# Optimization experiments

Measured on AMD Instinct MI355X. Metric: run time of the kernel, lower is better.

## Reference

```python
import jax, jax.numpy as jnp
import numpy as np

D_MODEL = 1024
N_HEAD = 16
HEAD_DIM = D_MODEL // N_HEAD


def setup_inputs() -> dict:
    key = jax.random.key(0)
    ks = jax.random.split(key, 11)
    B, S = 2, 2048
    scale = 1.0 / np.sqrt(D_MODEL)
    inp = {
        'q': jax.random.normal(ks[0], (B, S, D_MODEL), dtype=jnp.float32),
        'k': jax.random.normal(ks[1], (B, S, D_MODEL), dtype=jnp.float32),
        'v': jax.random.normal(ks[2], (B, S, D_MODEL), dtype=jnp.float32),
        'Wq': jax.random.normal(ks[3], (D_MODEL, D_MODEL), dtype=jnp.float32) * scale,
        'bq': jnp.zeros((D_MODEL,), dtype=jnp.float32),
        'Wk': jax.random.normal(ks[4], (D_MODEL, D_MODEL), dtype=jnp.float32) * scale,
        'bk': jnp.zeros((D_MODEL,), dtype=jnp.float32),
        'Wv': jax.random.normal(ks[5], (D_MODEL, D_MODEL), dtype=jnp.float32) * scale,
        'bv': jnp.zeros((D_MODEL,), dtype=jnp.float32),
        'Wo': jax.random.normal(ks[6], (D_MODEL, D_MODEL), dtype=jnp.float32) * scale,
        'bo': jnp.zeros((D_MODEL,), dtype=jnp.float32),
    }
    return inp


def _split_heads(x):
    # [B, S, D] -> [B, H, S, Dh]
    B, S, _ = x.shape
    return x.reshape(B, S, N_HEAD, HEAD_DIM).transpose(0, 2, 1, 3)


def reference(q, k, v, Wq, bq, Wk, bk, Wv, bv, Wo, bo):
    B, S, _ = q.shape
    qh = _split_heads(q @ Wq + bq)  # [B,H,S,Dh]
    kh = _split_heads(k @ Wk + bk)
    vh = _split_heads(v @ Wv + bv)
    inv_sqrt_d = jnp.asarray(1.0 / np.sqrt(HEAD_DIM), dtype=q.dtype)
    scores = jnp.einsum('bhqd,bhkd->bhqk', qh, kh) * inv_sqrt_d  # [B,H,S,S]
    attn = jax.nn.softmax(scores, axis=-1)
    out = jnp.einsum('bhqk,bhkd->bhqd', attn, vh)  # [B,H,S,Dh]
    out = out.transpose(0, 2, 1, 3).reshape(B, S, D_MODEL)
    return out @ Wo + bo
```

## Files before the change

kernel.cpp:

```cpp
#include <hip/hip_runtime.h>
#include <cstdint>
#include <cstddef>

#define D_MODEL 1024
#define NHEAD 16
#define HDIM 64
#define BATCH 2
#define SEQ 2048
#define MROWS (BATCH*SEQ)

typedef _Float16 f16;
typedef _Float16 f16x2 __attribute__((ext_vector_type(2)));
typedef _Float16 f16x4 __attribute__((ext_vector_type(4)));
typedef _Float16 f16x8 __attribute__((ext_vector_type(8)));
typedef float f32x4 __attribute__((ext_vector_type(4)));
typedef __fp16 fp16x2_raw __attribute__((ext_vector_type(2)));

__device__ __forceinline__ f16x2 cvt_pk(float a, float b) {
  fp16x2_raw t = __builtin_amdgcn_cvt_pkrtz(a, b);
  return __builtin_bit_cast(f16x2, t);
}

__device__ __forceinline__ float fast_exp2(float x) {
  return __builtin_amdgcn_exp2f(x);
}

#define QSCALE 0.18033688011112042f
#define CSHIFT 6.0f

__device__ __forceinline__ void gload_lds16(const void* gsrc, void* ldst) {
  __builtin_amdgcn_global_load_lds(
      (__attribute__((address_space(1))) void*)gsrc,
      (__attribute__((address_space(3))) void*)ldst,
      16, 0, 0);
}

__global__ __launch_bounds__(256) void cast3_kernel(
    const float* __restrict__ q, const float* __restrict__ k,
    const float* __restrict__ v, f16* __restrict__ Xf) {
  const int z = blockIdx.y;
  const float* in = (z == 0) ? q : (z == 1) ? k : v;
  f16* out = Xf + (size_t)z * MROWS * D_MODEL;
  int i = (blockIdx.x * 256 + threadIdx.x) * 8;
  const float4* p = (const float4*)(in + i);
  float4 a = p[0], b = p[1];
  f16x8 o = { (f16)a.x,(f16)a.y,(f16)a.z,(f16)a.w,
              (f16)b.x,(f16)b.y,(f16)b.z,(f16)b.w };
  *(f16x8*)(out + i) = o;
}

__global__ __launch_bounds__(256) void transpose4_kernel(
    const float* __restrict__ W0, const float* __restrict__ W1,
    const float* __restrict__ W2, const float* __restrict__ W3,
    f16* __restrict__ T0, f16* __restrict__ T1,
    f16* __restrict__ T2, f16* __restrict__ T3) {
  const int z = blockIdx.z;
  const float* W = (z == 0) ? W0 : (z == 1) ? W1 : (z == 2) ? W2 : W3;
  f16* Wt = (z == 0) ? T0 : (z == 1) ? T1 : (z == 2) ? T2 : T3;
  __shared__ float tile[32][33];
  int n0 = blockIdx.x * 32, k0 = blockIdx.y * 32;
  int tx = threadIdx.x, ty = threadIdx.y;
  #pragma unroll
  for (int j = 0; j < 32; j += 8)
    tile[ty + j][tx] = W[(size_t)(k0 + ty + j) * D_MODEL + n0 + tx];
  __syncthreads();
  #pragma unroll
  for (int j = 0; j < 32; j += 8)
    Wt[(size_t)(n0 + ty + j) * D_MODEL + k0 + tx] = (f16)tile[tx][ty + j];
}

__global__ __launch_bounds__(256, 3) void gemm_qkv(
    const f16* __restrict__ Xf,
    const f16* __restrict__ Wtq, const f16* __restrict__ Wtk, const f16* __restrict__ Wtv,
    const float* __restrict__ bq, const float* __restrict__ bk, const float* __restrict__ bv,
    f16* __restrict__ Qh, f16* __restrict__ Kf, f16* __restrict__ Vf) {
  __shared__ __align__(16) f16 As[128 * 64];
  __shared__ __align__(16) f16 Bs[128 * 64];
  const int id = blockIdx.x;
  const int xcd = id & 7;
  const int s5 = id >> 3;
  const int bn_i = s5 & 7;
  const int t5 = xcd * 12 + (s5 >> 3);
  const int z = t5 >> 5;
  const int bm_i = t5 & 31;
  const int bm = bm_i * 128, bn = bn_i * 128;
  const f16* A  = Xf + (size_t)z * MROWS * D_MODEL + (size_t)bm * 1024;
  const f16* Bt = ((z == 0) ? Wtq : (z == 1) ? Wtk : Wtv) + (size_t)bn * 1024;
  const float* bias = (z == 0) ? bq : (z == 1) ? bk : bv;
  const int tid = threadIdx.x, wave = tid >> 6, lane = tid & 63;
  const int lr = lane & 15, lq = lane >> 4, sw = lr & 7;
  const int wm = (wave >> 1) * 64, wn = (wave & 1) * 64;
  const int srow = lane >> 3;
  const int scs  = (lane & 7) ^ srow;
  const f16* Ag = A  + (size_t)(wave * 32 + srow) * 1024 + scs * 8;
  const f16* Bg = Bt + (size_t)(wave * 32 + srow) * 1024 + scs * 8;

  f32x4 acc[4][4];
  #pragma unroll
  for (int i = 0; i < 4; i++)
    #pragma unroll
    for (int j = 0; j < 4; j++) acc[i][j] = (f32x4){0.f, 0.f, 0.f, 0.f};

  for (int k0 = 0; k0 < 1024; k0 += 64) {
    __syncthreads();
    #pragma unroll
    for (int g = 0; g < 4; g++) {
      gload_lds16(Ag + (size_t)g * 8 * 1024 + k0, As + wave * 2048 + g * 512);
      gload_lds16(Bg + (size_t)g * 8 * 1024 + k0, Bs + wave * 2048 + g * 512);
    }
    __syncthreads();
    #pragma unroll
    for (int t = 0; t < 2; t++) {
      f16x8 af[4], bf[4];
      #pragma unroll
      for (int m = 0; m < 4; m++)
        af[m] = *(const f16x8*)(As + (size_t)(wm + m * 16 + lr) * 64 + (((t * 4 + lq) ^ sw) * 8));
      #pragma unroll
      for (int j = 0; j < 4; j++)
        bf[j] = *(const f16x8*)(Bs + (size_t)(wn + j * 16 + lr) * 64 + (((t * 4 + lq) ^ sw) * 8));
      #pragma unroll
      for (int m = 0; m < 4; m++)
        #pragma unroll
        for (int j = 0; j < 4; j++)
          acc[m][j] = __builtin_amdgcn_mfma_f32_16x16x32_f16(af[m], bf[j], acc[m][j], 0, 0, 0);
    }
  }

  #pragma unroll
  for (int j = 0; j < 4; j++) {
    const int col = bn + wn + j * 16 + lr;
    const float bj = bias[col];
    const int hh = col >> 6, d = col & 63;
    #pragma unroll
    for (int m = 0; m < 4; m++) {
      #pragma unroll
      for (int r = 0; r < 4; r++) {
        const int row = bm + wm + m * 16 + lq * 4 + r;
        float val = acc[m][j][r] + bj;
        if (z == 0) val *= QSCALE;
        const int b = row >> 11, s = row & 2047;
        const size_t bh = (size_t)b * NHEAD + hh;
        const int tile = s >> 6;
        if (z == 0) {
          Qh[(bh * SEQ + s) * HDIM + d] = (f16)val;
        } else if (z == 1) {
          const int kk = s & 63;
          const int f = ((kk >> 4) << 1) | (d >> 5);
          const int ln = ((d >> 3) & 3) * 16 + (kk & 15);
          Kf[((bh * 32 + tile) * 8 + f) * 512 + ln * 8 + (d & 7)] = (f16)val;
        } else {
          const int kp = (((s >> 4) & 1) << 5) | (((s >> 2) & 3) << 3)
                       | (((s >> 5) & 1) << 2) | (s & 3);
          const int f = ((d >> 4) << 1) | (kp >> 5);
          const int ln = ((kp >> 3) & 3) * 16 + (d & 15);
          Vf[((bh * 32 + tile) * 8 + f) * 512 + ln * 8 + (kp & 7)] = (f16)val;
        }
      }
    }
  }
}

__global__ __launch_bounds__(256, 4) void gemm_o(
    const f16* __restrict__ AO, const f16* __restrict__ Wto,
    const float* __restrict__ bo, float* __restrict__ out) {
  __shared__ __align__(16) f16 As[64 * 64];
  __shared__ __align__(16) f16 Bs[128 * 64];
  const int id = blockIdx.x;
  const int xcd = id & 7;
  const int s5 = id >> 3;
  const int bn_i = s5 & 7;
  const int bm_i = xcd * 8 + (s5 >> 3);
  const int bm = bm_i * 64, bn = bn_i * 128;
  const int tid = threadIdx.x, wave = tid >> 6, lane = tid & 63;
  const int lr = lane & 15, lq = lane >> 4, sw = lr & 7;
  const int wm = (wave >> 1) * 32, wn = (wave & 1) * 64;
  const int srow = lane >> 3;
  const int scs  = (lane & 7) ^ srow;
  const f16* Ag = AO  + (size_t)(bm + wave * 16 + srow) * 1024 + scs * 8;
  const f16* Bg = Wto + (size_t)(bn + wave * 32 + srow) * 1024 + scs * 8;

  f32x4 acc[2][4];
  #pragma unroll
  for (int i = 0; i < 2; i++)
    #pragma unroll
    for (int j = 0; j < 4; j++) acc[i][j] = (f32x4){0.f, 0.f, 0.f, 0.f};

  for (int k0 = 0; k0 < 1024; k0 += 64) {
    __syncthreads();
    #pragma unroll
    for (int g = 0; g < 2; g++)
      gload_lds16(Ag + (size_t)g * 8 * 1024 + k0, As + wave * 1024 + g * 512);
    #pragma unroll
    for (int g = 0; g < 4; g++)
      gload_lds16(Bg + (size_t)g * 8 * 1024 + k0, Bs + wave * 2048 + g * 512);
    __syncthreads();
    #pragma unroll
    for (int t = 0; t < 2; t++) {
      f16x8 af[2], bf[4];
      #pragma unroll
      for (int m = 0; m < 2; m++)
        af[m] = *(const f16x8*)(As + (size_t)(wm + m * 16 + lr) * 64 + (((t * 4 + lq) ^ sw) * 8));
      #pragma unroll
      for (int j = 0; j < 4; j++)
        bf[j] = *(const f16x8*)(Bs + (size_t)(wn + j * 16 + lr) * 64 + (((t * 4 + lq) ^ sw) * 8));
      #pragma unroll
      for (int m = 0; m < 2; m++)
        #pragma unroll
        for (int j = 0; j < 4; j++)
          acc[m][j] = __builtin_amdgcn_mfma_f32_16x16x32_f16(af[m], bf[j], acc[m][j], 0, 0, 0);
    }
  }
  #pragma unroll
  for (int j = 0; j < 4; j++) {
    const int col = bn + wn + j * 16 + lr;
    const float bj = bo[col];
    #pragma unroll
    for (int m = 0; m < 2; m++)
      #pragma unroll
      for (int r = 0; r < 4; r++) {
        const int row = bm + wm + m * 16 + lq * 4 + r;
        out[(size_t)row * D_MODEL + col] = acc[m][j][r] + bj;
      }
  }
}

__global__ __launch_bounds__(256, 2) void flash_kernel(
    const f16* __restrict__ Qh, const f16* __restrict__ Kf,
    const f16* __restrict__ Vf, f16* __restrict__ AO) {
  __shared__ __align__(16) f16 Ks[2][8 * 512];
  const int id = blockIdx.x;
  const int xcd = id & 7;
  const int s6 = id >> 3;
  const int q_i = s6 & 15;
  const int hl = xcd * 4 + (s6 >> 4);
  const int h = hl & 15, b = hl >> 4;
  const int tid = threadIdx.x, wave = tid >> 6, lane = tid & 63;
  const int lr = lane & 15, lq = lane >> 4;
  const size_t bh = (size_t)b * NHEAD + h;
  const f16* Qb = Qh + bh * SEQ * HDIM;
  const f16* Kb = Kf + bh * 32 * 4096 + lane * 8;
  const f16* Vb = Vf + bh * 32 * 4096 + lane * 8;
  const int q0 = q_i * 128 + wave * 32;

  f16x8 aq[2][2];
  #pragma unroll
  for (int m = 0; m < 2; m++)
    #pragma unroll
    for (int t = 0; t < 2; t++)
      aq[m][t] = *(const f16x8*)(Qb + (size_t)(q0 + m * 16 + lr) * HDIM + t * 32 + lq * 8);

  f32x4 oacc[2][4], ls[2];
  #pragma unroll
  for (int m = 0; m < 2; m++) {
    ls[m] = (f32x4){0.f, 0.f, 0.f, 0.f};
    #pragma unroll
    for (int j = 0; j < 4; j++) oacc[m][j] = (f32x4){0.f, 0.f, 0.f, 0.f};
  }
  const f32x4 mC = {-CSHIFT, -CSHIFT, -CSHIFT, -CSHIFT};
  const f16x8 ones = {(f16)1, (f16)1, (f16)1, (f16)1, (f16)1, (f16)1, (f16)1, (f16)1};

  #define FITER(it, CUR, PF, PVW)                                              \
    do {                                                                       \
      f16x8 vv[8];                                                             \
      _Pragma("unroll")                                                        \
      for (int f = 0; f < 8; f++)                                              \
        vv[f] = *(const f16x8*)(Vb + ((size_t)(it) * 8 + f) * 512);            \
      if (PF) {                                                                \
        gload_lds16(Kb + ((size_t)((it) + 1) * 8 + 2 * wave) * 512,            \
                    &Ks[(CUR) ^ 1][(2 * wave) * 512]);                         \
        gload_lds16(Kb + ((size_t)((it) + 1) * 8 + 2 * wave + 1) * 512,        \
                    &Ks[(CUR) ^ 1][(2 * wave + 1) * 512]);                     \
      }                                                                        \
      __builtin_amdgcn_sched_barrier(0);                                       \
      f32x4 sc[4][2];                                                          \
      _Pragma("unroll")                                                        \
      for (int t = 0; t < 2; t++) {                                            \
        f16x8 bk[4];                                                           \
        _Pragma("unroll")                                                      \
        for (int j = 0; j < 4; j++)                                            \
          bk[j] = *(const f16x8*)(&Ks[CUR][(j * 2 + t) * 512 + lane * 8]);     \
        _Pragma("unroll")                                                      \
        for (int j = 0; j < 4; j++)                                            \
          _Pragma("unroll")                                                    \
          for (int m = 0; m < 2; m++)                                          \
            sc[j][m] = __builtin_amdgcn_mfma_f32_16x16x32_f16(                 \
                bk[j], aq[m][t], (t == 0) ? mC : sc[j][m], 0, 0, 0);           \
      }                                                                        \
      f16x8 ap[2][2];                                                          \
      _Pragma("unroll")                                                        \
      for (int m = 0; m < 2; m++)                                              \
        _Pragma("unroll")                                                      \
        for (int t = 0; t < 2; t++) {                                          \
          union { f16x8 v; f16x2 h2[4]; } u;                                   \
          const f32x4 lo = sc[t][m], hi = sc[t + 2][m];                        \
          u.h2[0] = cvt_pk(fast_exp2(lo[0]), fast_exp2(lo[1]));                \
          u.h2[1] = cvt_pk(fast_exp2(lo[2]), fast_exp2(lo[3]));                \
          u.h2[2] = cvt_pk(fast_exp2(hi[0]), fast_exp2(hi[1]));                \
          u.h2[3] = cvt_pk(fast_exp2(hi[2]), fast_exp2(hi[3]));                \
          ap[m][t] = u.v;                                                      \
        }                                                                      \
      asm volatile("s_waitcnt vmcnt(" #PVW ")" ::: "memory");                  \
      __builtin_amdgcn_sched_barrier(0);                                       \
      _Pragma("unroll")                                                        \
      for (int t = 0; t < 2; t++) {                                            \
        _Pragma("unroll")                                                      \
        for (int j = 0; j < 4; j++)                                            \
          _Pragma("unroll")                                                    \
          for (int m = 0; m < 2; m++)                                          \
            oacc[m][j] = __builtin_amdgcn_mfma_f32_16x16x32_f16(               \
                ap[m][t], vv[j * 2 + t], oacc[m][j], 0, 0, 0);                 \
        _Pragma("unroll")                                                      \
        for (int m = 0; m < 2; m++)                                            \
          ls[m] = __builtin_amdgcn_mfma_f32_16x16x32_f16(                      \
              ap[m][t], ones, ls[m], 0, 0, 0);                                 \
      }                                                                        \
      if (PF) {                                                                \
        asm volatile("s_waitcnt vmcnt(0)" ::: "memory");                       \
        __builtin_amdgcn_s_barrier();                                          \
        __builtin_amdgcn_sched_barrier(0);                                     \
      }                                                                        \
    } while (0)

  gload_lds16(Kb + (size_t)(2 * wave) * 512, &Ks[0][(2 * wave) * 512]);
  gload_lds16(Kb + (size_t)(2 * wave + 1) * 512, &Ks[0][(2 * wave + 1) * 512]);
  __syncthreads();

  for (int it2 = 0; it2 < 15; it2++) {
    FITER(it2 * 2,     0, 1, 2);
    FITER(it2 * 2 + 1, 1, 1, 2);
  }
  FITER(30, 0, 1, 2);
  FITER(31, 1, 0, 0);
  #undef FITER

  #pragma unroll
  for (int m = 0; m < 2; m++)
    #pragma unroll
    for (int r = 0; r < 4; r++) {
      const float inv = 1.0f / ls[m][r];
      const int row = q0 + m * 16 + lq * 4 + r;
      #pragma unroll
      for (int j = 0; j < 4; j++) {
        const int col = h * HDIM + j * 16 + lr;
        AO[((size_t)b * SEQ + row) * D_MODEL + col] = (f16)(oacc[m][j][r] * inv);
      }
    }
}

extern "C" void kernel_launch(void* const* d_in, const int* in_sizes, int n_in,
                              void* d_out, int out_size, void* d_ws, size_t ws_size,
                              hipStream_t stream) {
  const float* q  = (const float*)d_in[0];
  const float* k  = (const float*)d_in[1];
  const float* v  = (const float*)d_in[2];
  const float* Wq = (const float*)d_in[3];
  const float* bq = (const float*)d_in[4];
  const float* Wk = (const float*)d_in[5];
  const float* bk = (const float*)d_in[6];
  const float* Wv = (const float*)d_in[7];
  const float* bv = (const float*)d_in[8];
  const float* Wo = (const float*)d_in[9];
  const float* bo = (const float*)d_in[10];
  float* out = (float*)d_out;

  char* ws = (char*)d_ws;
  f16* Wt_q = (f16*)(ws + ((size_t)0  << 20));
  f16* Wt_k = (f16*)(ws + ((size_t)2  << 20));
  f16* Wt_v = (f16*)(ws + ((size_t)4  << 20));
  f16* Wt_o = (f16*)(ws + ((size_t)6  << 20));
  f16* Xf   = (f16*)(ws + ((size_t)8  << 20));
  f16* Qh_  = (f16*)(ws + ((size_t)32 << 20));
  f16* Kf_  = (f16*)(ws + ((size_t)40 << 20));
  f16* Vf_  = (f16*)(ws + ((size_t)48 << 20));
  f16* AO   = Xf;

  transpose4_kernel<<<dim3(32, 32, 4), dim3(32, 8), 0, stream>>>(
      Wq, Wk, Wv, Wo, Wt_q, Wt_k, Wt_v, Wt_o);

  cast3_kernel<<<dim3(2048, 3), 256, 0, stream>>>(q, k, v, Xf);

  gemm_qkv<<<768, 256, 0, stream>>>(
      Xf, Wt_q, Wt_k, Wt_v, bq, bk, bv, Qh_, Kf_, Vf_);

  flash_kernel<<<512, 256, 0, stream>>>(Qh_, Kf_, Vf_, AO);

  gemm_o<<<512, 256, 0, stream>>>(AO, Wt_o, bo, out);
}
```

Measured before the change: 205.4 us.

## Split flash attention KV range across two wave groups with LDS reduction

The flash kernel now runs 512 threads per block: two groups of four waves each process half of the key/value sequence for the same 128 query rows, with a separate double-buffered K tile per group. At the end, the partial output accumulators and row sums from the second group are passed through shared memory in two rounds and added by the first group, which then normalizes and writes the output. This is meant to double the waves available per block and halve the serial KV loop length to improve latency hiding. In exchange it adds LDS traffic, extra barriers for the reduction, and higher register and occupancy pressure under launch_bounds(512,4). Merging by plain addition is only correct because the kernel uses a fixed exponent shift rather than a running max.

After: 321.9 us. 1.57x slower.

```diff
diff --git a/kernel.cpp b/kernel.cpp
--- a/kernel.cpp
+++ b/kernel.cpp
@@ -224,10 +224,10 @@
   }
 }
 
-__global__ __launch_bounds__(256, 2) void flash_kernel(
+__global__ __launch_bounds__(512, 4) void flash_kernel(
     const f16* __restrict__ Qh, const f16* __restrict__ Kf,
     const f16* __restrict__ Vf, f16* __restrict__ AO) {
-  __shared__ __align__(16) f16 Ks[2][8 * 512];
+  __shared__ __align__(16) f16 Ks[2][2][8 * 512];
   const int id = blockIdx.x;
   const int xcd = id & 7;
   const int s6 = id >> 3;
@@ -235,12 +235,14 @@
   const int hl = xcd * 4 + (s6 >> 4);
   const int h = hl & 15, b = hl >> 4;
   const int tid = threadIdx.x, wave = tid >> 6, lane = tid & 63;
+  const int pr = wave >> 2;
+  const int sq = wave & 3;
   const int lr = lane & 15, lq = lane >> 4;
   const size_t bh = (size_t)b * NHEAD + h;
   const f16* Qb = Qh + bh * SEQ * HDIM;
   const f16* Kb = Kf + bh * 32 * 4096 + lane * 8;
   const f16* Vb = Vf + bh * 32 * 4096 + lane * 8;
-  const int q0 = q_i * 128 + wave * 32;
+  const int q0 = q_i * 128 + sq * 32;
 
   f16x8 aq[2][2];
   #pragma unroll
@@ -261,15 +263,16 @@
 
   #define FITER(it, CUR, PF, PVW)                                              \
     do {                                                                       \
+      const int gt = pr * 16 + (it);                                           \
       f16x8 vv[8];                                                             \
       _Pragma("unroll")                                                        \
       for (int f = 0; f < 8; f++)                                              \
-        vv[f] = *(const f16x8*)(Vb + ((size_t)(it) * 8 + f) * 512);            \
+        vv[f] = *(const f16x8*)(Vb + ((size_t)gt * 8 + f) * 512);              \
       if (PF) {                                                                \
-        gload_lds16(Kb + ((size_t)((it) + 1) * 8 + 2 * wave) * 512,            \
-                    &Ks[(CUR) ^ 1][(2 * wave) * 512]);                         \
-        gload_lds16(Kb + ((size_t)((it) + 1) * 8 + 2 * wave + 1) * 512,        \
-                    &Ks[(CUR) ^ 1][(2 * wave + 1) * 512]);                     \
+        gload_lds16(Kb + ((size_t)(gt + 1) * 8 + 2 * sq) * 512,                \
+                    &Ks[pr][(CUR) ^ 1][(2 * sq) * 512]);                       \
+        gload_lds16(Kb + ((size_t)(gt + 1) * 8 + 2 * sq + 1) * 512,            \
+                    &Ks[pr][(CUR) ^ 1][(2 * sq + 1) * 512]);                   \
       }                                                                        \
       __builtin_amdgcn_sched_barrier(0);                                       \
       f32x4 sc[4][2];                                                          \
@@ -278,7 +281,7 @@
         f16x8 bk[4];                                                           \
         _Pragma("unroll")                                                      \
         for (int j = 0; j < 4; j++)                                            \
-          bk[j] = *(const f16x8*)(&Ks[CUR][(j * 2 + t) * 512 + lane * 8]);     \
+          bk[j] = *(const f16x8*)(&Ks[pr][CUR][(j * 2 + t) * 512 + lane * 8]); \
         _Pragma("unroll")                                                      \
         for (int j = 0; j < 4; j++)                                            \
           _Pragma("unroll")                                                    \
@@ -321,30 +324,63 @@
       }                                                                        \
     } while (0)
 
-  gload_lds16(Kb + (size_t)(2 * wave) * 512, &Ks[0][(2 * wave) * 512]);
-  gload_lds16(Kb + (size_t)(2 * wave + 1) * 512, &Ks[0][(2 * wave + 1) * 512]);
+  gload_lds16(Kb + ((size_t)(pr * 16) * 8 + 2 * sq) * 512,
+              &Ks[pr][0][(2 * sq) * 512]);
+  gload_lds16(Kb + ((size_t)(pr * 16) * 8 + 2 * sq + 1) * 512,
+              &Ks[pr][0][(2 * sq + 1) * 512]);
   __syncthreads();
 
-  for (int it2 = 0; it2 < 15; it2++) {
-    FITER(it2 * 2,     0, 1, 2);
-    FITER(it2 * 2 + 1, 1, 1, 2);
-  }
-  FITER(30, 0, 1, 2);
-  FITER(31, 1, 0, 0);
+  for (int i2 = 0; i2 < 7; i2++) {
+    FITER(i2 * 2,     0, 1, 2);
+    FITER(i2 * 2 + 1, 1, 1, 2);
+  }
+  FITER(14, 0, 1, 2);
+  FITER(15, 1, 0, 0);
   #undef FITER
 
-  #pragma unroll
-  for (int m = 0; m < 2; m++)
-    #pragma unroll
-    for (int r = 0; r < 4; r++) {
-      const float inv = 1.0f / ls[m][r];
-      const int row = q0 + m * 16 + lq * 4 + r;
-      #pragma unroll
-      for (int j = 0; j < 4; j++) {
-        const int col = h * HDIM + j * 16 + lr;
-        AO[((size_t)b * SEQ + row) * D_MODEL + col] = (f16)(oacc[m][j][r] * inv);
+  __syncthreads();
+  {
+    float* C0 = (float*)&Ks[0][0][0];
+    #pragma unroll
+    for (int rnd = 0; rnd < 2; rnd++) {
+      const int wsl = sq - rnd * 2;
+      if (pr == 1 && (sq >> 1) == rnd) {
+        float* slot = C0 + wsl * 2560;
+        #pragma unroll
+        for (int m = 0; m < 2; m++)
+          #pragma unroll
+          for (int j = 0; j < 4; j++)
+            *(f32x4*)(slot + (m * 4 + j) * 256 + lane * 4) = oacc[m][j];
+        #pragma unroll
+        for (int m = 0; m < 2; m++)
+          *(f32x4*)(slot + 2048 + m * 256 + lane * 4) = ls[m];
       }
+      __syncthreads();
+      if (pr == 0 && (sq >> 1) == rnd) {
+        float* slot = C0 + wsl * 2560;
+        #pragma unroll
+        for (int m = 0; m < 2; m++) {
+          ls[m] += *(const f32x4*)(slot + 2048 + m * 256 + lane * 4);
+          #pragma unroll
+          for (int j = 0; j < 4; j++)
+            oacc[m][j] += *(const f32x4*)(slot + (m * 4 + j) * 256 + lane * 4);
+        }
+        #pragma unroll
+        for (int m = 0; m < 2; m++)
+          #pragma unroll
+          for (int r = 0; r < 4; r++) {
+            const float inv = 1.0f / ls[m][r];
+            const int row = q0 + m * 16 + lq * 4 + r;
+            #pragma unroll
+            for (int j = 0; j < 4; j++) {
+              const int col = h * HDIM + j * 16 + lr;
+              AO[((size_t)b * SEQ + row) * D_MODEL + col] = (f16)(oacc[m][j][r] * inv);
+            }
+          }
+      }
+      __syncthreads();
     }
+  }
 }
 
 extern "C" void kernel_launch(void* const* d_in, const int* in_sizes, int n_in,
@@ -382,7 +418,7 @@
   gemm_qkv<<<768, 256, 0, stream>>>(
       Xf, Wt_q, Wt_k, Wt_v, bq, bk, bv, Qh_, Kf_, Vf_);
 
-  flash_kernel<<<512, 256, 0, stream>>>(Qh_, Kf_, Vf_, AO);
+  flash_kernel<<<512, 512, 0, stream>>>(Qh_, Kf_, Vf_, AO);
 
   gemm_o<<<512, 256, 0, stream>>>(AO, Wt_o, bo, out);
 }
```
